# Kernel tuning notes

Hardware: AMD Instinct MI355X
Metric: run time of the kernel (lower is better)

Reference implementation:

```python
import jax, jax.numpy as jnp
import numpy as np

IN_C, HID, N_NODES, WINDOW = 8, 64, 20000, 8
N_BIG = N_NODES * WINDOW          # 160000 supernodes (window-stacked graph)
E, E_DEC = 1_600_000, 500_000
EPS = 1e-5
DH = 2 * HID + IN_C + WINDOW - 1  # 143, decoder hidden size


def _gcn(x, row, col, ew, W, b, n):
    # GCNConv with self-loops + symmetric normalization (PyG semantics)
    loop = jnp.arange(n)
    r = jnp.concatenate([row, loop])
    c = jnp.concatenate([col, loop])
    w = jnp.concatenate([ew, jnp.ones((n,), ew.dtype)])
    deg = jax.ops.segment_sum(w, c, num_segments=n)
    dis = jnp.where(deg > 0, jax.lax.rsqrt(jnp.maximum(deg, EPS)), 0.0)
    norm = dis[r] * w * dis[c]
    h = x @ W                                  # [n, HID]
    agg = jax.ops.segment_sum(norm[:, None] * h[r], c, num_segments=n)
    return agg + b


def _bn(x, g, be):
    # BatchNorm1d, training-mode batch statistics (biased var)
    m = x.mean(0)
    v = x.var(0)
    return (x - m) * jax.lax.rsqrt(v + EPS) * g + be


def _lstm(X, Wih, Whh, bih, bhh):
    # X: [T, B, F]; PyTorch gate order i,f,g,o
    Hd = Whh.shape[1]
    B = X.shape[1]

    def step(carry, xt):
        h, c = carry
        gates = xt @ Wih.T + h @ Whh.T + bih + bhh
        i, f, g, o = jnp.split(gates, 4, axis=-1)
        c = jax.nn.sigmoid(f) * c + jax.nn.sigmoid(i) * jnp.tanh(g)
        h = jax.nn.sigmoid(o) * jnp.tanh(c)
        return (h, c), h

    init = (jnp.zeros((B, Hd), X.dtype), jnp.zeros((B, Hd), X.dtype))
    (h, _), ys = jax.lax.scan(step, init, X)
    return ys, h


def setup_inputs() -> dict:
    key = jax.random.key(0)
    ks = jax.random.split(key, 20)
    f32 = jnp.float32
    sc = lambda k, shape, fan: (jax.random.normal(k, shape, f32) / np.sqrt(fan)).astype(f32)
    d = {}
    d["x"] = jax.random.normal(ks[0], (N_BIG, IN_C), f32)
    d["edge_attr"] = jax.random.uniform(ks[1], (E,), f32)
    d["edge_index"] = jax.random.randint(ks[2], (2, E), 0, N_BIG)
    d["edge_weights_index"] = jax.random.randint(ks[3], (2, E_DEC), 0, N_NODES)
    # GCN layer 1 and 2
    d["W1"] = sc(ks[4], (IN_C, HID), IN_C); d["b1"] = jnp.zeros((HID,), f32)
    d["g1"] = jnp.ones((HID,), f32); d["be1"] = jnp.zeros((HID,), f32)
    d["W2"] = sc(ks[5], (HID, HID), HID); d["b2"] = jnp.zeros((HID,), f32)
    d["g2"] = jnp.ones((HID,), f32); d["be2"] = jnp.zeros((HID,), f32)
    # LSTM 1 (input 2*HID) and LSTM 2 (input HID)
    d["Wih1"] = sc(ks[6], (4 * HID, 2 * HID), 2 * HID)
    d["Whh1"] = sc(ks[7], (4 * HID, HID), HID)
    d["bih1"] = jnp.zeros((4 * HID,), f32); d["bhh1"] = jnp.zeros((4 * HID,), f32)
    d["Wih2"] = sc(ks[8], (4 * HID, HID), HID)
    d["Whh2"] = sc(ks[9], (4 * HID, HID), HID)
    d["bih2"] = jnp.zeros((4 * HID,), f32); d["bhh2"] = jnp.zeros((4 * HID,), f32)
    # Edge decoder MLP
    d["dWa"] = sc(ks[10], (2 * DH, DH), 2 * DH); d["dba"] = jnp.zeros((DH,), f32)
    d["dWb"] = sc(ks[11], (DH, 1), DH); d["dbb"] = jnp.zeros((1,), f32)
    return d


def reference(x, edge_attr, W1, b1, g1, be1, W2, b2, g2, be2,
              Wih1, Whh1, bih1, bhh1, Wih2, Whh2, bih2, bhh2,
              dWa, dba, dWb, dbb, edge_index, edge_weights_index):
    row, col = edge_index[0], edge_index[1]
    # skip features S: first timestep full features + last channel of later steps
    Sx = x.reshape(WINDOW, N_NODES, IN_C).transpose(1, 0, 2)   # [N, W, C]
    S = jnp.concatenate([Sx[:, 0, :], Sx[:, 1:, IN_C - 1]], axis=1)  # [N, C+W-1]
    # two GCN layers (relu -> batchnorm; dropout identity in eval)
    h1 = _bn(jax.nn.relu(_gcn(x, row, col, edge_attr, W1, b1, N_BIG)), g1, be1)
    h2 = _bn(jax.nn.relu(_gcn(h1, row, col, edge_attr, W2, b2, N_BIG)), g2, be2)
    Xc = jnp.concatenate([h1, h2], axis=1).reshape(WINDOW, N_NODES, 2 * HID)
    y1, H1 = _lstm(Xc, Wih1, Whh1, bih1, bhh1)
    _, H2 = _lstm(y1, Wih2, Whh2, bih2, bhh2)
    node_emb = jnp.concatenate([H1, H2, S], axis=1)  # [N_NODES, DH]
    # edge decoder: gather-concat-MLP
    src, trg = edge_weights_index[0], edge_weights_index[1]
    ee = jnp.concatenate([node_emb[src], node_emb[trg]], axis=1)  # [E_DEC, 2*DH]
    h = jax.nn.relu(ee @ dWa + dba)
    return (h @ dWb + dbb).reshape(-1)
```

## Files before the change

### kernel.cpp

```cpp
#include <hip/hip_runtime.h>
#include <hip/hip_bf16.h>

#define IN_C 8
#define HID 64
#define N_NODES 20000
#define WINDOW 8
#define N_BIG 160000
#define NE 1600000
#define E_DEC 500000
#define DHV 143
#define EPSV 1e-5f
#define CAP 32
#define OVF_CAP 4096

typedef __hip_bfloat16 bf;
typedef __attribute__((ext_vector_type(8))) short short8;
typedef __attribute__((ext_vector_type(4))) float float4_;

__device__ __forceinline__ float b2f(bf v) { return __bfloat162float(v); }
__device__ __forceinline__ bf f2b(float v) { return __float2bfloat16(v); }
__device__ __forceinline__ float bflo(unsigned int u) { return __uint_as_float(u << 16); }
__device__ __forceinline__ float bfhi(unsigned int u) { return __uint_as_float(u & 0xffff0000u); }
__device__ __forceinline__ unsigned int packbf2(float lo, float hi) {
    unsigned int ul = __bfloat16_as_ushort(f2b(lo));
    unsigned int uh = __bfloat16_as_ushort(f2b(hi));
    return ul | (uh << 16);
}
__device__ __forceinline__ float sigf(float x) {
    return __builtin_amdgcn_rcpf(1.f + __expf(-x));
}
__device__ __forceinline__ float tanhfast(float x) {
    x = fminf(fmaxf(x, -15.f), 15.f);
    float e = __expf(2.f * x);
    return (e - 1.f) * __builtin_amdgcn_rcpf(e + 1.f);
}

__global__ void k_prep(const float* Wih2, const float* Whh2, const float* bih1, const float* bhh1,
                       const float* bih2, const float* bhh2, const float* dWa,
                       int* cnt, int* ovfn, bf* B2f, float* bc1, float* bc2, bf* Bpqf, float* stats)
{
    int i0 = blockIdx.x * blockDim.x + threadIdx.x;
    int stride = gridDim.x * blockDim.x;
    for (int i = i0; i < N_BIG; i += stride) cnt[i] = 0;
    if (i0 == 0) *ovfn = 0;
    for (int i = i0; i < 16 * 4 * 64 * 8; i += stride) {
        int j = i & 7, lane = (i >> 3) & 63, r = i >> 9;
        int c = r & 3, ct = r >> 2;
        int q = lane >> 4, l15 = lane & 15;
        int n = ct * 16 + l15, k = c * 32 + q * 8 + j;
        B2f[i] = f2b((k < 64) ? Wih2[n * 64 + k] : Whh2[n * 64 + (k - 64)]);
    }
    for (int i = i0; i < 256; i += stride) {
        bc1[i] = bih1[i] + bhh1[i];
        bc2[i] = bih2[i] + bhh2[i];
    }
    for (int i = i0; i < 18 * 5 * 64 * 8; i += stride) {
        int j = i & 7, lane = (i >> 3) & 63, r = i >> 9;
        int c = r % 5, ct = r / 5;
        int q = lane >> 4, l15 = lane & 15;
        int n = ct * 16 + l15, k = c * 32 + q * 8 + j;
        float v = 0.f;
        if (k < DHV) {
            if (n < DHV) v = dWa[k * DHV + n];
            else if (n >= 144 && n < 144 + DHV) v = dWa[(DHV + k) * DHV + (n - 144)];
        }
        Bpqf[i] = f2b(v);
    }
    for (int i = i0; i < 256; i += stride) stats[i] = 0.f;
}

__global__ __launch_bounds__(256) void k_fill_xw1(const int* ei, const float* ea,
                                                  const float* x, const float* W1,
                                                  int* cnt, float2* bucket, int* ovfn, float4* ovf,
                                                  bf* hbufb) {
    __shared__ float Ws[IN_C * HID];
    __shared__ float xs[4][IN_C];
    int tid = threadIdx.x;
    if (blockIdx.x < 6250) {
        int e = blockIdx.x * 256 + tid;
        int r = ei[e], c = ei[NE + e];
        float a = ea[e];
        int p = atomicAdd(&cnt[c], 1);
        if (p < CAP) bucket[(size_t)c * CAP + p] = make_float2(__int_as_float(r), a);
        else {
            int q = atomicAdd(ovfn, 1);
            if (q < OVF_CAP) ovf[q] = make_float4(__int_as_float(c), __int_as_float(r), a, 0.f);
        }
    } else {
        int bid = blockIdx.x - 6250;
        Ws[tid] = W1[tid];
        Ws[tid + 256] = W1[tid + 256];
        int node0 = bid * 4;
        if (tid < 32) xs[tid >> 3][tid & 7] = x[node0 * IN_C + tid];
        __syncthreads();
        int ch = tid & 63, ns = tid >> 6;
        float acc = 0.f;
#pragma unroll
        for (int c = 0; c < IN_C; c++) acc += xs[ns][c] * Ws[c * 64 + ch];
        hbufb[(size_t)(node0 + ns) * 64 + ch] = f2b(acc);
    }
}

__global__ __launch_bounds__(256) void k_disscale(const int* cnt, const float2* bucket,
                                                  const int* ovfn, const float4* ovf,
                                                  float* dis, bf* h) {
    int wv = (blockIdx.x * blockDim.x + threadIdx.x) >> 6;
    int half = (threadIdx.x >> 5) & 1, l = threadIdx.x & 31;
    int c = wv * 2 + half;
    if (c >= N_BIG) return;
    int n = cnt[c];
    int nb = (n < CAP) ? n : CAP;
    float s = 0.f;
    for (int i = l; i < nb; i += 32) s += bucket[(size_t)c * CAP + i].y;
    if (n > CAP) {
        int m = *ovfn; if (m > OVF_CAP) m = OVF_CAP;
        for (int i = l; i < m; i += 32) {
            float4 v = ovf[i];
            if (__float_as_int(v.x) == c) s += v.z;
        }
    }
#pragma unroll
    for (int off = 16; off > 0; off >>= 1) s += __shfl_xor(s, off);
    float deg = 1.f + s;
    float dv = rsqrtf(fmaxf(deg, EPSV));
    if (l == 0) dis[c] = dv;
    unsigned int hv = *(const unsigned int*)(h + (size_t)c * 64 + 2 * l);
    *(unsigned int*)(h + (size_t)c * 64 + 2 * l) = packbf2(dv * bflo(hv), dv * bfhi(hv));
}

__global__ void k_gcn_gather(const bf* h, const float* dis, const int* cnt,
                             const float2* bucket, const int* ovfn, const float4* ovf,
                             const float* bias, bf* outb) {
    int wv = (blockIdx.x * blockDim.x + threadIdx.x) >> 6;
    int half = (threadIdx.x >> 5) & 1, l = threadIdx.x & 31;
    int c = wv * 2 + half;
    if (c >= N_BIG) return;
    unsigned int hv = *(const unsigned int*)(h + (size_t)c * 64 + 2 * l);
    float ax = bflo(hv), ay = bfhi(hv);
    size_t o = (size_t)c * CAP;
    int nfull = cnt[c];
    int n = (nfull < CAP) ? nfull : CAP;
    int e = 0;
    for (; e + 8 <= n; e += 8) {
        float2 p[8];
#pragma unroll
        for (int j = 0; j < 8; j++) p[j] = bucket[o + e + j];
        unsigned int v[8];
#pragma unroll
        for (int j = 0; j < 8; j++)
            v[j] = *(const unsigned int*)(h + (size_t)__float_as_int(p[j].x) * 64 + 2 * l);
#pragma unroll
        for (int j = 0; j < 8; j++) { ax += p[j].y * bflo(v[j]); ay += p[j].y * bfhi(v[j]); }
    }
    for (; e + 4 <= n; e += 4) {
        float2 p[4];
#pragma unroll
        for (int j = 0; j < 4; j++) p[j] = bucket[o + e + j];
        unsigned int v[4];
#pragma unroll
        for (int j = 0; j < 4; j++)
            v[j] = *(const unsigned int*)(h + (size_t)__float_as_int(p[j].x) * 64 + 2 * l);
#pragma unroll
        for (int j = 0; j < 4; j++) { ax += p[j].y * bflo(v[j]); ay += p[j].y * bfhi(v[j]); }
    }
    for (; e < n; e++) {
        float2 p = bucket[o + e];
        unsigned int v = *(const unsigned int*)(h + (size_t)__float_as_int(p.x) * 64 + 2 * l);
        ax += p.y * bflo(v);
        ay += p.y * bfhi(v);
    }
    if (nfull > CAP) {
        int m = *ovfn; if (m > OVF_CAP) m = OVF_CAP;
        for (int i = 0; i < m; i++) {
            float4 v = ovf[i];
            if (__float_as_int(v.x) == c) {
                unsigned int hw = *(const unsigned int*)(h + (size_t)__float_as_int(v.y) * 64 + 2 * l);
                ax += v.z * bflo(hw);
                ay += v.z * bfhi(hw);
            }
        }
    }
    float dv = dis[c];
    float2 bv = *(const float2*)(bias + 2 * l);
    unsigned int st = packbf2(fmaxf(dv * ax + bv.x, 0.f), fmaxf(dv * ay + bv.y, 0.f));
    *(unsigned int*)(outb + (size_t)c * 64 + 2 * l) = st;
}

__global__ void k_bnstats(const bf* buf, float* s_sum, float* s_sq) {
    int ch = threadIdx.x & 63, g = threadIdx.x >> 6;
    float s = 0.f, q = 0.f;
    for (int r = blockIdx.x * 4 + g; r < N_BIG; r += gridDim.x * 4) {
        float v = b2f(buf[(size_t)r * 64 + ch]);
        s += v;
        q += v * v;
    }
    unsafeAtomicAdd(&s_sum[ch], s);
    unsafeAtomicAdd(&s_sq[ch], q);
}

__global__ __launch_bounds__(256) void k_fold1(const float* W2, const float* g1, const float* be1,
                                               const float* stats, bf* W2t, float* w2b, float* AC) {
    __shared__ float A[64], C[64];
    int tid = threadIdx.x;
    if (tid < 64) {
        float m = stats[tid] * (1.f / (float)N_BIG);
        float var = stats[64 + tid] * (1.f / (float)N_BIG) - m * m;
        float a = g1[tid] * rsqrtf(var + EPSV);
        float c = be1[tid] - m * a;
        A[tid] = a; C[tid] = c;
        AC[tid] = a; AC[64 + tid] = c;
    }
    __syncthreads();
    for (int i = tid; i < 4096; i += 256) {
        int n = i >> 6, k = i & 63;
        W2t[i] = f2b(W2[k * 64 + n] * A[k]);
    }
    if (tid < 64) {
        float s = 0.f;
        for (int k = 0; k < 64; k++) s += C[k] * W2[k * 64 + tid];
        w2b[tid] = s;
    }
}

__global__ void k_fold2(const float* Wih1, const float* Whh1,
                        const float* g2, const float* be2, const float* stats,
                        const float* AC, const float* bc1, bf* B1f, float* bc1f) {
    int i0 = blockIdx.x * blockDim.x + threadIdx.x;
    int stride = gridDim.x * blockDim.x;
    for (int i = i0; i < 16 * 6 * 64 * 8; i += stride) {
        int j = i & 7, lane = (i >> 3) & 63, r = i >> 9;
        int c = r % 6, ct = r / 6;
        int q = lane >> 4, l15 = lane & 15;
        int n = ct * 16 + l15, k = c * 32 + q * 8 + j;
        float w = (k < 128) ? Wih1[n * 128 + k] : Whh1[n * 64 + (k - 128)];
        float scale = 1.f;
        if (k < 64) scale = AC[k];
        else if (k < 128) {
            int ch = k - 64;
            float m = stats[128 + ch] * (1.f / (float)N_BIG);
            float var = stats[192 + ch] * (1.f / (float)N_BIG) - m * m;
            scale = g2[ch] * rsqrtf(var + EPSV);
        }
        B1f[i] = f2b(w * scale);
    }
    for (int n = i0; n < 256; n += stride) {
        float s = bc1[n];
        for (int k = 0; k < 64; k++) s += AC[64 + k] * Wih1[n * 128 + k];
        for (int ch = 0; ch < 64; ch++) {
            float m = stats[128 + ch] * (1.f / (float)N_BIG);
            float var = stats[192 + ch] * (1.f / (float)N_BIG) - m * m;
            float a = g2[ch] * rsqrtf(var + EPSV);
            float c2v = be2[ch] - m * a;
            s += c2v * Wih1[n * 128 + 64 + ch];
        }
        bc1f[n] = s;
    }
}

__global__ __launch_bounds__(256) void k_h1w2(const bf* h1b, const bf* W2t, const float* w2b,
                                              const float* dis, bf* outb) {
    int tid = threadIdx.x, w = tid >> 6, lane = tid & 63;
    int q = lane >> 4, l15 = lane & 15;
    size_t r0 = (size_t)blockIdx.x * 64 + w * 16;
    float4_ acc[4];
#pragma unroll
    for (int ct = 0; ct < 4; ct++) acc[ct] = (float4_){0.f, 0.f, 0.f, 0.f};
#pragma unroll
    for (int c = 0; c < 2; c++) {
        int koff = c * 32 + q * 8;
        short8 a = *(const short8*)(h1b + (r0 + l15) * 64 + koff);
#pragma unroll
        for (int ct = 0; ct < 4; ct++) {
            short8 b = *(const short8*)(W2t + (size_t)(ct * 16 + l15) * 64 + koff);
            acc[ct] = __builtin_amdgcn_mfma_f32_16x16x32_bf16(a, b, acc[ct], 0, 0, 0);
        }
    }
    size_t node0 = r0 + q * 4;
#pragma unroll
    for (int reg = 0; reg < 4; reg++) {
        float dv = dis[node0 + reg];
#pragma unroll
        for (int ct = 0; ct < 4; ct++)
            outb[(node0 + reg) * 64 + ct * 16 + l15] = f2b(dv * (acc[ct][reg] + w2b[ct * 16 + l15]));
    }
}

__global__ __launch_bounds__(256, 1) void k_lstm_fused(
    const bf* h1b, const bf* h2b, const bf* B1f, const bf* B2f,
    const float* bc1, const float* bc2, bf* H1out, bf* H2out)
{
    __shared__ bf h1s[2][32][72];
    __shared__ bf h2s[2][32][72];
    int tid = threadIdx.x, w = tid >> 6, lane = tid & 63;
    int q = lane >> 4, l15 = lane & 15;
    int gnode0 = blockIdx.x * 32;
    short8 B1r[6][4];
    short8 B2r[4][4];
#pragma unroll
    for (int c = 0; c < 6; c++)
#pragma unroll
        for (int g = 0; g < 4; g++)
            B1r[c][g] = *(const short8*)(B1f + (size_t)(((w + 4 * g) * 6 + c) * 64 + lane) * 8);
#pragma unroll
    for (int c = 0; c < 4; c++)
#pragma unroll
        for (int g = 0; g < 4; g++)
            B2r[c][g] = *(const short8*)(B2f + (size_t)(((w + 4 * g) * 4 + c) * 64 + lane) * 8);
    float c1[2][4] = {}, c2[2][4] = {};
    float bv1[4], bv2[4];
#pragma unroll
    for (int g = 0; g < 4; g++) {
        bv1[g] = bc1[(w + 4 * g) * 16 + l15];
        bv2[g] = bc2[(w + 4 * g) * 16 + l15];
    }
    short8 Ag[4][2], An[4][2];
#pragma unroll
    for (int c = 0; c < 4; c++) {
        const bf* sp = (c < 2) ? h1b : h2b;
        int koff = (c & 1) * 32 + q * 8;
#pragma unroll
        for (int m = 0; m < 2; m++)
            Ag[c][m] = *(const short8*)(sp + (size_t)(gnode0 + m * 16 + l15) * 64 + koff);
    }
#pragma unroll
    for (int t = 0; t < WINDOW; t++) {
        int cur = t & 1, prv = cur ^ 1;
        float4_ acc[2][4];
#pragma unroll
        for (int m = 0; m < 2; m++)
#pragma unroll
            for (int g = 0; g < 4; g++) acc[m][g] = (float4_){bv1[g], bv1[g], bv1[g], bv1[g]};
#pragma unroll
        for (int c = 0; c < 4; c++)
#pragma unroll
            for (int m = 0; m < 2; m++)
#pragma unroll
                for (int g = 0; g < 4; g++)
                    acc[m][g] = __builtin_amdgcn_mfma_f32_16x16x32_bf16(Ag[c][m], B1r[c][g], acc[m][g], 0, 0, 0);
        if (t < WINDOW - 1) {
            const size_t toff2 = (size_t)(t + 1) * N_NODES * 64;
#pragma unroll
            for (int c = 0; c < 4; c++) {
                const bf* sp = (c < 2) ? h1b + toff2 : h2b + toff2;
                int koff = (c & 1) * 32 + q * 8;
#pragma unroll
                for (int m = 0; m < 2; m++)
                    An[c][m] = *(const short8*)(sp + (size_t)(gnode0 + m * 16 + l15) * 64 + koff);
            }
        }
        if (t > 0) {
#pragma unroll
            for (int c = 4; c < 6; c++) {
                int koff = (c & 1) * 32 + q * 8;
#pragma unroll
                for (int m = 0; m < 2; m++) {
                    short8 a = *(const short8*)&h1s[prv][m * 16 + l15][koff];
#pragma unroll
                    for (int g = 0; g < 4; g++)
                        acc[m][g] = __builtin_amdgcn_mfma_f32_16x16x32_bf16(a, B1r[c][g], acc[m][g], 0, 0, 0);
                }
            }
        }
#pragma unroll
        for (int m = 0; m < 2; m++)
#pragma unroll
            for (int reg = 0; reg < 4; reg++) {
                float gi = acc[m][0][reg], gf = acc[m][1][reg];
                float gg = acc[m][2][reg], go = acc[m][3][reg];
                float co = (t == 0) ? 0.f : c1[m][reg];
                float cn = sigf(gf) * co + sigf(gi) * tanhfast(gg);
                float hn = sigf(go) * tanhfast(cn);
                c1[m][reg] = cn;
                int nl = m * 16 + q * 4 + reg;
                h1s[cur][nl][w * 16 + l15] = f2b(hn);
                if (t == WINDOW - 1)
                    H1out[(size_t)(gnode0 + nl) * 64 + w * 16 + l15] = f2b(hn);
            }
        __syncthreads();
#pragma unroll
        for (int m = 0; m < 2; m++)
#pragma unroll
            for (int g = 0; g < 4; g++) acc[m][g] = (float4_){bv2[g], bv2[g], bv2[g], bv2[g]};
#pragma unroll
        for (int c = 0; c < 2; c++) {
            int koff = (c & 1) * 32 + q * 8;
#pragma unroll
            for (int m = 0; m < 2; m++) {
                short8 a = *(const short8*)&h1s[cur][m * 16 + l15][koff];
#pragma unroll
                for (int g = 0; g < 4; g++)
                    acc[m][g] = __builtin_amdgcn_mfma_f32_16x16x32_bf16(a, B2r[c][g], acc[m][g], 0, 0, 0);
            }
        }
        if (t > 0) {
#pragma unroll
            for (int c = 2; c < 4; c++) {
                int koff = (c & 1) * 32 + q * 8;
#pragma unroll
                for (int m = 0; m < 2; m++) {
                    short8 a = *(const short8*)&h2s[prv][m * 16 + l15][koff];
#pragma unroll
                    for (int g = 0; g < 4; g++)
                        acc[m][g] = __builtin_amdgcn_mfma_f32_16x16x32_bf16(a, B2r[c][g], acc[m][g], 0, 0, 0);
                }
            }
        }
#pragma unroll
        for (int m = 0; m < 2; m++)
#pragma unroll
            for (int reg = 0; reg < 4; reg++) {
                float gi = acc[m][0][reg], gf = acc[m][1][reg];
                float gg = acc[m][2][reg], go = acc[m][3][reg];
                float co = (t == 0) ? 0.f : c2[m][reg];
                float cn = sigf(gf) * co + sigf(gi) * tanhfast(gg);
                float hn = sigf(go) * tanhfast(cn);
                c2[m][reg] = cn;
                int nl = m * 16 + q * 4 + reg;
                h2s[cur][nl][w * 16 + l15] = f2b(hn);
                if (t == WINDOW - 1)
                    H2out[(size_t)(gnode0 + nl) * 64 + w * 16 + l15] = f2b(hn);
            }
        __syncthreads();
#pragma unroll
        for (int c = 0; c < 4; c++)
#pragma unroll
            for (int m = 0; m < 2; m++) Ag[c][m] = An[c][m];
    }
}

__global__ void k_nodeemb(const bf* H1, const bf* H2, const float* x, bf* neb) {
    int stride = gridDim.x * blockDim.x;
    for (int idx = blockIdx.x * blockDim.x + threadIdx.x; idx < N_NODES * 160; idx += stride) {
        int n = idx / 160, j = idx % 160;
        float v;
        if (j < 64) v = b2f(H1[(size_t)n * 64 + j]);
        else if (j < 128) v = b2f(H2[(size_t)n * 64 + (j - 64)]);
        else if (j < DHV) {
            int s = j - 128;
            v = (s < 8) ? x[n * IN_C + s] : x[(size_t)((s - 7) * N_NODES + n) * IN_C + 7];
        } else v = 0.f;
        neb[idx] = f2b(v);
    }
}

__global__ __launch_bounds__(256) void k_pq(const bf* neb, const bf* Bpqf, const float* dba, bf* PQb) {
    int tid = threadIdx.x, w = tid >> 6, lane = tid & 63;
    int q = lane >> 4, l15 = lane & 15;
    int r0 = blockIdx.x * 64 + w * 16;
    float4_ acc[18];
#pragma unroll
    for (int ct = 0; ct < 18; ct++) acc[ct] = (float4_){0.f, 0.f, 0.f, 0.f};
#pragma unroll
    for (int c = 0; c < 5; c++) {
        short8 a = *(const short8*)(neb + (size_t)(r0 + l15) * 160 + c * 32 + q * 8);
#pragma unroll
        for (int ct = 0; ct < 18; ct++) {
            short8 b = *(const short8*)(Bpqf + (size_t)((ct * 5 + c) * 64 + lane) * 8);
            acc[ct] = __builtin_amdgcn_mfma_f32_16x16x32_bf16(a, b, acc[ct], 0, 0, 0);
        }
    }
#pragma unroll
    for (int reg = 0; reg < 4; reg++) {
        int node = r0 + q * 4 + reg;
        if (node < N_NODES)
#pragma unroll
            for (int ct = 0; ct < 18; ct++) {
                int col = ct * 16 + l15;
                float add = (ct < 9 && col < DHV) ? dba[col] : 0.f;
                PQb[(size_t)node * 288 + col] = f2b(acc[ct][reg] + add);
            }
    }
}

__global__ __launch_bounds__(256) void k_edge(const int* ewi, const bf* PQb,
                                              const float* dWb, const float* dbb, float* out) {
    int wv = (blockIdx.x * blockDim.x + threadIdx.x) >> 6;
    int half = (threadIdx.x >> 5) & 1, l = threadIdx.x & 31;
    int e = wv * 2 + half;
    if (e >= E_DEC) return;
    int src = ewi[e], trg = ewi[E_DEC + e];
    const bf* Pr = PQb + (size_t)src * 288;
    const bf* Qr = PQb + (size_t)trg * 288 + 144;
    float acc;
    {
        uint2 pv = *(const uint2*)(Pr + 4 * l);
        uint2 qv = *(const uint2*)(Qr + 4 * l);
        float4 wv4 = *(const float4*)(dWb + 4 * l);
        float s0 = fmaxf(bflo(pv.x) + bflo(qv.x), 0.f);
        float s1 = fmaxf(bfhi(pv.x) + bfhi(qv.x), 0.f);
        float s2 = fmaxf(bflo(pv.y) + bflo(qv.y), 0.f);
        float s3 = fmaxf(bfhi(pv.y) + bfhi(qv.y), 0.f);
        acc = s0 * wv4.x + s1 * wv4.y + s2 * wv4.z + s3 * wv4.w;
    }
    if (l < 4) {
        int u0 = 128 + 4 * l;
        uint2 pv = *(const uint2*)(Pr + u0);
        uint2 qv = *(const uint2*)(Qr + u0);
        float w0 = dWb[u0], w1 = dWb[u0 + 1], w2 = dWb[u0 + 2];
        float w3 = (u0 + 3 < DHV) ? dWb[u0 + 3] : 0.f;
        acc += fmaxf(bflo(pv.x) + bflo(qv.x), 0.f) * w0;
        acc += fmaxf(bfhi(pv.x) + bfhi(qv.x), 0.f) * w1;
        acc += fmaxf(bflo(pv.y) + bflo(qv.y), 0.f) * w2;
        acc += fmaxf(bfhi(pv.y) + bfhi(qv.y), 0.f) * w3;
    }
#pragma unroll
    for (int off = 16; off > 0; off >>= 1) acc += __shfl_xor(acc, off);
    if (l == 0) out[e] = acc + dbb[0];
}

extern "C" void kernel_launch(void* const* d_in, const int* in_sizes, int n_in,
                              void* d_out, int out_size, void* d_ws, size_t ws_size,
                              hipStream_t stream) {
    (void)in_sizes; (void)n_in; (void)out_size; (void)ws_size;
    const float* x    = (const float*)d_in[0];
    const float* ea   = (const float*)d_in[1];
    const int*   ei   = (const int*)d_in[2];
    const int*   ewi  = (const int*)d_in[3];
    const float* W1   = (const float*)d_in[4];
    const float* b1   = (const float*)d_in[5];
    const float* g1   = (const float*)d_in[6];
    const float* be1  = (const float*)d_in[7];
    const float* W2   = (const float*)d_in[8];
    const float* b2   = (const float*)d_in[9];
    const float* g2   = (const float*)d_in[10];
    const float* be2  = (const float*)d_in[11];
    const float* Wih1 = (const float*)d_in[12];
    const float* Whh1 = (const float*)d_in[13];
    const float* bih1 = (const float*)d_in[14];
    const float* bhh1 = (const float*)d_in[15];
    const float* Wih2 = (const float*)d_in[16];
    const float* Whh2 = (const float*)d_in[17];
    const float* bih2 = (const float*)d_in[18];
    const float* bhh2 = (const float*)d_in[19];
    const float* dWa  = (const float*)d_in[20];
    const float* dba  = (const float*)d_in[21];
    const float* dWb  = (const float*)d_in[22];
    const float* dbb  = (const float*)d_in[23];
    float* out = (float*)d_out;

    const size_t NSB = (size_t)N_BIG * 64;
    const size_t NS  = (size_t)N_NODES * 64;
    char* base = (char*)d_ws;
    size_t o = 0;
    float* dis  = (float*)(base + o); o += (size_t)N_BIG * 4;
    bf* aggb    = (bf*)(base + o);    o += NSB * 2;
    bf* hbufb   = (bf*)(base + o);    o += NSB * 2;
    bf* h1b     = (bf*)(base + o);    o += NSB * 2;
    bf* h2b     = (bf*)(base + o);    o += NSB * 2;
    bf* hs1     = (bf*)(base + o);    o += NS * 2;
    bf* hs2     = (bf*)(base + o);    o += NS * 2;
    bf* B1f     = (bf*)(base + o);    o += (size_t)16 * 6 * 64 * 8 * 2;
    bf* B2f     = (bf*)(base + o);    o += (size_t)16 * 4 * 64 * 8 * 2;
    bf* W2t     = (bf*)(base + o);    o += 64 * 64 * 2;
    float* bc1  = (float*)(base + o); o += 256 * 4;
    float* bc2  = (float*)(base + o); o += 256 * 4;
    bf* Bpqf    = (bf*)(base + o);    o += (size_t)18 * 5 * 64 * 8 * 2;
    float* stats= (float*)(base + o); o += 256 * 4;
    float* w2b  = (float*)(base + o); o += 64 * 4;
    float* AC   = (float*)(base + o); o += 128 * 4;
    float* bc1f = (float*)(base + o); o += 256 * 4;
    int* cnt    = (int*)(base + o);   o += (size_t)N_BIG * 4;
    int* ovfn   = (int*)(base + o);   o += 256;
    float4* ovf = (float4*)(base + o); o += (size_t)OVF_CAP * 16;
    float2* bucket = (float2*)(base + o); o += (size_t)N_BIG * CAP * 8;
    bf* neb = aggb;
    bf* PQb = aggb + (size_t)20032 * 160;

    k_prep<<<512, 256, 0, stream>>>(Wih2, Whh2, bih1, bhh1, bih2, bhh2, dWa,
                                    cnt, ovfn, B2f, bc1, bc2, Bpqf, stats);
    k_fill_xw1<<<6250 + 40000, 256, 0, stream>>>(ei, ea, x, W1, cnt, bucket, ovfn, ovf, hbufb);
    k_disscale<<<N_BIG / 8, 256, 0, stream>>>(cnt, bucket, ovfn, ovf, dis, hbufb);

    k_gcn_gather<<<N_BIG / 8, 256, 0, stream>>>(hbufb, dis, cnt, bucket, ovfn, ovf, b1, h1b);
    k_bnstats<<<256, 256, 0, stream>>>(h1b, stats, stats + 64);
    k_fold1<<<1, 256, 0, stream>>>(W2, g1, be1, stats, W2t, w2b, AC);

    k_h1w2<<<2500, 256, 0, stream>>>(h1b, W2t, w2b, dis, hbufb);
    k_gcn_gather<<<N_BIG / 8, 256, 0, stream>>>(hbufb, dis, cnt, bucket, ovfn, ovf, b2, h2b);
    k_bnstats<<<256, 256, 0, stream>>>(h2b, stats + 128, stats + 192);
    k_fold2<<<64, 256, 0, stream>>>(Wih1, Whh1, g2, be2, stats, AC, bc1, B1f, bc1f);

    k_lstm_fused<<<625, 256, 0, stream>>>(h1b, h2b, B1f, B2f, bc1f, bc2, hs1, hs2);

    k_nodeemb<<<12500, 256, 0, stream>>>(hs1, hs2, x, neb);
    k_pq<<<313, 256, 0, stream>>>(neb, Bpqf, dba, PQb);
    k_edge<<<E_DEC / 8, 256, 0, stream>>>(ewi, PQb, dWb, dbb, out);
}
```

Before: 688.3 us.

## Fuse BN stats into GCN gather, node-emb build into PQ GEMM, split fill kernel

BatchNorm sum and sum-of-squares are now reduced per block inside the GCN gather kernel and written as partials, then summed by a small deterministic reduction kernel. This replaces the separate pass that reread the activations and used atomics. The node-embedding concat is built directly in shared memory inside the PQ GEMM kernel, so the intermediate buffer and its kernel go away. The combined edge-fill/xW1 kernel is split into two launches. The trade-offs are an extra __syncthreads in the gather, a 10 MB partials buffer, and loss of overlap between the fill and xW1 work.

```diff
diff --git a/kernel.cpp b/kernel.cpp
--- a/kernel.cpp
+++ b/kernel.cpp
@@ -12,6 +12,7 @@
 #define EPSV 1e-5f
 #define CAP 32
 #define OVF_CAP 4096
+#define NER 168
 
 typedef __hip_bfloat16 bf;
 typedef __attribute__((ext_vector_type(8))) short short8;
@@ -69,36 +70,33 @@
     for (int i = i0; i < 256; i += stride) stats[i] = 0.f;
 }
 
-__global__ __launch_bounds__(256) void k_fill_xw1(const int* ei, const float* ea,
-                                                  const float* x, const float* W1,
-                                                  int* cnt, float2* bucket, int* ovfn, float4* ovf,
-                                                  bf* hbufb) {
+__global__ __launch_bounds__(256) void k_fill(const int* ei, const float* ea,
+                                              int* cnt, float2* bucket, int* ovfn, float4* ovf) {
+    int e = blockIdx.x * 256 + threadIdx.x;
+    int r = ei[e], c = ei[NE + e];
+    float a = ea[e];
+    int p = atomicAdd(&cnt[c], 1);
+    if (p < CAP) bucket[(size_t)c * CAP + p] = make_float2(__int_as_float(r), a);
+    else {
+        int q = atomicAdd(ovfn, 1);
+        if (q < OVF_CAP) ovf[q] = make_float4(__int_as_float(c), __int_as_float(r), a, 0.f);
+    }
+}
+
+__global__ __launch_bounds__(256) void k_xw1(const float* x, const float* W1, bf* hbufb) {
     __shared__ float Ws[IN_C * HID];
     __shared__ float xs[4][IN_C];
     int tid = threadIdx.x;
-    if (blockIdx.x < 6250) {
-        int e = blockIdx.x * 256 + tid;
-        int r = ei[e], c = ei[NE + e];
-        float a = ea[e];
-        int p = atomicAdd(&cnt[c], 1);
-        if (p < CAP) bucket[(size_t)c * CAP + p] = make_float2(__int_as_float(r), a);
-        else {
-            int q = atomicAdd(ovfn, 1);
-            if (q < OVF_CAP) ovf[q] = make_float4(__int_as_float(c), __int_as_float(r), a, 0.f);
-        }
-    } else {
-        int bid = blockIdx.x - 6250;
-        Ws[tid] = W1[tid];
-        Ws[tid + 256] = W1[tid + 256];
-        int node0 = bid * 4;
-        if (tid < 32) xs[tid >> 3][tid & 7] = x[node0 * IN_C + tid];
-        __syncthreads();
-        int ch = tid & 63, ns = tid >> 6;
-        float acc = 0.f;
-#pragma unroll
-        for (int c = 0; c < IN_C; c++) acc += xs[ns][c] * Ws[c * 64 + ch];
-        hbufb[(size_t)(node0 + ns) * 64 + ch] = f2b(acc);
-    }
+    Ws[tid] = W1[tid];
+    Ws[tid + 256] = W1[tid + 256];
+    int node0 = blockIdx.x * 4;
+    if (tid < 32) xs[tid >> 3][tid & 7] = x[node0 * IN_C + tid];
+    __syncthreads();
+    int ch = tid & 63, ns = tid >> 6;
+    float acc = 0.f;
+#pragma unroll
+    for (int c = 0; c < IN_C; c++) acc += xs[ns][c] * Ws[c * 64 + ch];
+    hbufb[(size_t)(node0 + ns) * 64 + ch] = f2b(acc);
 }
 
 __global__ __launch_bounds__(256) void k_disscale(const int* cnt, const float2* bucket,
@@ -128,13 +126,14 @@
     *(unsigned int*)(h + (size_t)c * 64 + 2 * l) = packbf2(dv * bflo(hv), dv * bfhi(hv));
 }
 
-__global__ void k_gcn_gather(const bf* h, const float* dis, const int* cnt,
+__global__ __launch_bounds__(256) void k_gcn_gather(const bf* h, const float* dis, const int* cnt,
                              const float2* bucket, const int* ovfn, const float4* ovf,
-                             const float* bias, bf* outb) {
-    int wv = (blockIdx.x * blockDim.x + threadIdx.x) >> 6;
-    int half = (threadIdx.x >> 5) & 1, l = threadIdx.x & 31;
+                             const float* bias, bf* outb, float* part) {
+    __shared__ float4 red[256];
+    int tid = threadIdx.x;
+    int wv = (blockIdx.x * 256 + tid) >> 6;
+    int half = (tid >> 5) & 1, l = tid & 31;
     int c = wv * 2 + half;
-    if (c >= N_BIG) return;
     unsigned int hv = *(const unsigned int*)(h + (size_t)c * 64 + 2 * l);
     float ax = bflo(hv), ay = bfhi(hv);
     size_t o = (size_t)c * CAP;
@@ -182,20 +181,35 @@
     }
     float dv = dis[c];
     float2 bv = *(const float2*)(bias + 2 * l);
-    unsigned int st = packbf2(fmaxf(dv * ax + bv.x, 0.f), fmaxf(dv * ay + bv.y, 0.f));
-    *(unsigned int*)(outb + (size_t)c * 64 + 2 * l) = st;
-}
-
-__global__ void k_bnstats(const bf* buf, float* s_sum, float* s_sq) {
-    int ch = threadIdx.x & 63, g = threadIdx.x >> 6;
-    float s = 0.f, q = 0.f;
-    for (int r = blockIdx.x * 4 + g; r < N_BIG; r += gridDim.x * 4) {
-        float v = b2f(buf[(size_t)r * 64 + ch]);
-        s += v;
-        q += v * v;
-    }
-    unsafeAtomicAdd(&s_sum[ch], s);
-    unsafeAtomicAdd(&s_sq[ch], q);
+    float vx = fmaxf(dv * ax + bv.x, 0.f);
+    float vy = fmaxf(dv * ay + bv.y, 0.f);
+    *(unsigned int*)(outb + (size_t)c * 64 + 2 * l) = packbf2(vx, vy);
+    red[tid] = make_float4(vx, vy, vx * vx, vy * vy);
+    __syncthreads();
+    if (tid < 32) {
+        float4 s = make_float4(0.f, 0.f, 0.f, 0.f);
+#pragma unroll
+        for (int i = 0; i < 8; i++) {
+            float4 v = red[((i >> 1) << 6) + ((i & 1) << 5) + tid];
+            s.x += v.x; s.y += v.y; s.z += v.z; s.w += v.w;
+        }
+        float* pb = part + (size_t)blockIdx.x * 128;
+        pb[2 * tid] = s.x; pb[2 * tid + 1] = s.y;
+        pb[64 + 2 * tid] = s.z; pb[64 + 2 * tid + 1] = s.w;
+    }
+}
+
+__global__ __launch_bounds__(256) void k_bnred(const float* part, int nblk, float* stats_out) {
+    __shared__ float s[256];
+    float acc = 0.f;
+    for (int b = threadIdx.x; b < nblk; b += 256) acc += part[(size_t)b * 128 + blockIdx.x];
+    s[threadIdx.x] = acc;
+    __syncthreads();
+    for (int off = 128; off; off >>= 1) {
+        if (threadIdx.x < off) s[threadIdx.x] += s[threadIdx.x + off];
+        __syncthreads();
+    }
+    if (threadIdx.x == 0) stats_out[blockIdx.x] = s[0];
 }
 
 __global__ __launch_bounds__(256) void k_fold1(const float* W2, const float* g1, const float* be1,
@@ -428,31 +442,40 @@
     }
 }
 
-__global__ void k_nodeemb(const bf* H1, const bf* H2, const float* x, bf* neb) {
-    int stride = gridDim.x * blockDim.x;
-    for (int idx = blockIdx.x * blockDim.x + threadIdx.x; idx < N_NODES * 160; idx += stride) {
-        int n = idx / 160, j = idx % 160;
-        float v;
-        if (j < 64) v = b2f(H1[(size_t)n * 64 + j]);
-        else if (j < 128) v = b2f(H2[(size_t)n * 64 + (j - 64)]);
-        else if (j < DHV) {
-            int s = j - 128;
-            v = (s < 8) ? x[n * IN_C + s] : x[(size_t)((s - 7) * N_NODES + n) * IN_C + 7];
-        } else v = 0.f;
-        neb[idx] = f2b(v);
-    }
-}
-
-__global__ __launch_bounds__(256) void k_pq(const bf* neb, const bf* Bpqf, const float* dba, bf* PQb) {
+__global__ __launch_bounds__(256) void k_pq(const bf* H1, const bf* H2, const float* x,
+                                            const bf* Bpqf, const float* dba, bf* PQb) {
+    __shared__ bf ne[64][NER];
     int tid = threadIdx.x, w = tid >> 6, lane = tid & 63;
     int q = lane >> 4, l15 = lane & 15;
-    int r0 = blockIdx.x * 64 + w * 16;
+    int r0 = blockIdx.x * 64;
+    for (int i = tid; i < 64 * 16; i += 256) {
+        int rr = i >> 4, cc = (i & 15) * 4;
+        int gr = r0 + rr;
+        uint2 v1 = make_uint2(0u, 0u), v2 = make_uint2(0u, 0u);
+        if (gr < N_NODES) {
+            v1 = *(const uint2*)(H1 + (size_t)gr * 64 + cc);
+            v2 = *(const uint2*)(H2 + (size_t)gr * 64 + cc);
+        }
+        *(uint2*)&ne[rr][cc] = v1;
+        *(uint2*)&ne[rr][64 + cc] = v2;
+    }
+    for (int i = tid; i < 64 * 32; i += 256) {
+        int rr = i >> 5, cc = 128 + (i & 31);
+        int gr = r0 + rr;
+        float v = 0.f;
+        if (gr < N_NODES && cc < DHV) {
+            int s = cc - 128;
+            v = (s < 8) ? x[gr * IN_C + s] : x[(size_t)((s - 7) * N_NODES + gr) * IN_C + 7];
+        }
+        ne[rr][cc] = f2b(v);
+    }
+    __syncthreads();
     float4_ acc[18];
 #pragma unroll
     for (int ct = 0; ct < 18; ct++) acc[ct] = (float4_){0.f, 0.f, 0.f, 0.f};
 #pragma unroll
     for (int c = 0; c < 5; c++) {
-        short8 a = *(const short8*)(neb + (size_t)(r0 + l15) * 160 + c * 32 + q * 8);
+        short8 a = *(const short8*)&ne[w * 16 + l15][c * 32 + q * 8];
 #pragma unroll
         for (int ct = 0; ct < 18; ct++) {
             short8 b = *(const short8*)(Bpqf + (size_t)((ct * 5 + c) * 64 + lane) * 8);
@@ -461,13 +484,15 @@
     }
 #pragma unroll
     for (int reg = 0; reg < 4; reg++) {
-        int node = r0 + q * 4 + reg;
-        if (node < N_NODES)
+        int node = r0 + w * 16 + 0;
+        int nrow = r0 + w * 16 + q * 4 + reg;
+        (void)node;
+        if (nrow < N_NODES)
 #pragma unroll
             for (int ct = 0; ct < 18; ct++) {
                 int col = ct * 16 + l15;
                 float add = (ct < 9 && col < DHV) ? dba[col] : 0.f;
-                PQb[(size_t)node * 288 + col] = f2b(acc[ct][reg] + add);
+                PQb[(size_t)nrow * 288 + col] = f2b(acc[ct][reg] + add);
             }
     }
 }
@@ -543,7 +568,7 @@
     char* base = (char*)d_ws;
     size_t o = 0;
     float* dis  = (float*)(base + o); o += (size_t)N_BIG * 4;
-    bf* aggb    = (bf*)(base + o);    o += NSB * 2;
+    bf* PQb     = (bf*)(base + o);    o += NSB * 2;
     bf* hbufb   = (bf*)(base + o);    o += NSB * 2;
     bf* h1b     = (bf*)(base + o);    o += NSB * 2;
     bf* h2b     = (bf*)(base + o);    o += NSB * 2;
@@ -563,26 +588,25 @@
     int* ovfn   = (int*)(base + o);   o += 256;
     float4* ovf = (float4*)(base + o); o += (size_t)OVF_CAP * 16;
     float2* bucket = (float2*)(base + o); o += (size_t)N_BIG * CAP * 8;
-    bf* neb = aggb;
-    bf* PQb = aggb + (size_t)20032 * 160;
+    float* part = (float*)(base + o); o += (size_t)20000 * 128 * 4;
 
     k_prep<<<512, 256, 0, stream>>>(Wih2, Whh2, bih1, bhh1, bih2, bhh2, dWa,
                                     cnt, ovfn, B2f, bc1, bc2, Bpqf, stats);
-    k_fill_xw1<<<6250 + 40000, 256, 0, stream>>>(ei, ea, x, W1, cnt, bucket, ovfn, ovf, hbufb);
+    k_fill<<<6250, 256, 0, stream>>>(ei, ea, cnt, bucket, ovfn, ovf);
+    k_xw1<<<N_BIG / 4, 256, 0, stream>>>(x, W1, hbufb);
     k_disscale<<<N_BIG / 8, 256, 0, stream>>>(cnt, bucket, ovfn, ovf, dis, hbufb);
 
-    k_gcn_gather<<<N_BIG / 8, 256, 0, stream>>>(hbufb, dis, cnt, bucket, ovfn, ovf, b1, h1b);
-    k_bnstats<<<256, 256, 0, stream>>>(h1b, stats, stats + 64);
+    k_gcn_gather<<<N_BIG / 8, 256, 0, stream>>>(hbufb, dis, cnt, bucket, ovfn, ovf, b1, h1b, part);
+    k_bnred<<<128, 256, 0, stream>>>(part, 20000, stats);
     k_fold1<<<1, 256, 0, stream>>>(W2, g1, be1, stats, W2t, w2b, AC);
 
     k_h1w2<<<2500, 256, 0, stream>>>(h1b, W2t, w2b, dis, hbufb);
-    k_gcn_gather<<<N_BIG / 8, 256, 0, stream>>>(hbufb, dis, cnt, bucket, ovfn, ovf, b2, h2b);
-    k_bnstats<<<256, 256, 0, stream>>>(h2b, stats + 128, stats + 192);
+    k_gcn_gather<<<N_BIG / 8, 256, 0, stream>>>(hbufb, dis, cnt, bucket, ovfn, ovf, b2, h2b, part);
+    k_bnred<<<128, 256, 0, stream>>>(part, 20000, stats + 128);
     k_fold2<<<64, 256, 0, stream>>>(Wih1, Whh1, g2, be2, stats, AC, bc1, B1f, bc1f);
 
     k_lstm_fused<<<625, 256, 0, stream>>>(h1b, h2b, B1f, B2f, bc1f, bc2, hs1, hs2);
 
-    k_nodeemb<<<12500, 256, 0, stream>>>(hs1, hs2, x, neb);
-    k_pq<<<313, 256, 0, stream>>>(neb, Bpqf, dba, PQb);
+    k_pq<<<313, 256, 0, stream>>>(hs1, hs2, x, Bpqf, dba, PQb);
     k_edge<<<E_DEC / 8, 256, 0, stream>>>(ewi, PQb, dWb, dbb, out);
 }
```

Measured after the change: 638.9 us. -7.2%, faster.
